# Performance work log

Measured on AMD Instinct MI355X. Metric: run time of the kernel, lower is better.

## Reference

```python
import jax, jax.numpy as jnp
import numpy as np

F_IN = 512
N_STAGES = 6
BATCH = 16384


def entmax15_1d(v):
    # Exact entmax with alpha=1.5 on a 1D vector (Peters et al. 2019).
    x = (v - jnp.max(v)) * 0.5
    xs = jnp.sort(x)[::-1]                      # descending
    rho = jnp.arange(1, xs.shape[0] + 1, dtype=xs.dtype)
    mean = jnp.cumsum(xs) / rho
    mean_sq = jnp.cumsum(xs * xs) / rho
    ss = rho * (mean_sq - mean * mean)
    delta = jnp.clip((1.0 - ss) / rho, 0.0, None)
    tau = mean - jnp.sqrt(delta)
    support_size = jnp.sum(tau <= xs)
    tau_star = tau[support_size - 1]
    return jnp.square(jnp.clip(x - tau_star, 0.0, None))


def setup_inputs() -> dict:
    key = jax.random.key(0)
    ks = jax.random.split(key, 7)
    F2 = 2 * F_IN
    lim_in = 1.0 / np.sqrt(F2)   # torch Linear default init bound (fan_in = 2F)
    x = jax.random.normal(ks[0], (BATCH, F_IN), dtype=jnp.float32)
    masks = jax.random.uniform(ks[1], (N_STAGES, F_IN), dtype=jnp.float32)  # Beta-sampled in torch; uniform(0,1) is in-range
    Win_w = jax.random.uniform(ks[2], (N_STAGES, F2, F2), minval=-lim_in, maxval=lim_in, dtype=jnp.float32)
    Win_b = jax.random.uniform(ks[3], (N_STAGES, F2), minval=-lim_in, maxval=lim_in, dtype=jnp.float32)
    Wout_w = jax.random.uniform(ks[4], (N_STAGES, F_IN, F2), minval=-lim_in, maxval=lim_in, dtype=jnp.float32)
    Wout_b = jax.random.uniform(ks[5], (N_STAGES, F_IN), minval=-lim_in, maxval=lim_in, dtype=jnp.float32)
    return {"x": x, "masks": masks, "Win_w": Win_w, "Win_b": Win_b,
            "Wout_w": Wout_w, "Wout_b": Wout_b}


def reference(x, masks, Win_w, Win_b, Wout_w, Wout_b):
    F = x.shape[-1]
    h = x
    for d in range(N_STAGES):
        feature = entmax15_1d(masks[d]) * x                      # [B, F]
        h_in = jnp.concatenate([feature, h], axis=-1) @ Win_w[d].T + Win_b[d]  # [B, 2F]
        z = jax.nn.sigmoid(h_in[:, :F])
        r = jax.nn.sigmoid(h_in[:, F:])
        h_out = jnp.tanh(jnp.concatenate([r * h, x], axis=-1) @ Wout_w[d].T + Wout_b[d])
        h = (1.0 - z) * h + z * h_out                            # dropout p=0 -> identity
    return h
```

## Files before the change

### kernel.cpp

```cpp
#include <hip/hip_runtime.h>
#include <stdint.h>
#include <math.h>

typedef unsigned short u16;
typedef short s16x8 __attribute__((ext_vector_type(8)));
typedef float f32x4 __attribute__((ext_vector_type(4)));
typedef u16 u16x4 __attribute__((ext_vector_type(4)));

#define FDIM 512
#define F2 1024
#define BATCH 16384
#define NST 6
#define KDIM 1024
#define NT 32

__device__ __forceinline__ u16 f2bf(float f) {
  uint32_t u = __float_as_uint(f);
  u += 0x7FFFu + ((u >> 16) & 1u);
  return (u16)(u >> 16);
}
__device__ __forceinline__ float bf2f(u16 b) {
  return __uint_as_float((uint32_t)b << 16);
}

#define LOG2E 1.44269504f
__device__ __forceinline__ float fast_sigmoid(float v) {
  float e = __builtin_amdgcn_exp2f(-v * LOG2E);
  return __builtin_amdgcn_rcpf(1.0f + e);
}
__device__ __forceinline__ float fast_tanh(float v) {
  float e = __builtin_amdgcn_exp2f(v * (2.0f * LOG2E));
  return 1.0f - 2.0f * __builtin_amdgcn_rcpf(1.0f + e);
}

__device__ __forceinline__ void ld_lds16(u16* lds, const u16* g) {
  __builtin_amdgcn_global_load_lds(
      (const __attribute__((address_space(1))) uint32_t*)g,
      (__attribute__((address_space(3))) uint32_t*)lds, 16, 0, 0);
}

__global__ __launch_bounds__(512) void entmax_kernel(const float* __restrict__ masks,
                                                     float* __restrict__ fm) {
  __shared__ float sx[FDIM];
  __shared__ float ssort[FDIM];
  __shared__ float stau[FDIM];
  __shared__ float2 sc[2][FDIM];
  const int d = blockIdx.x;
  const int j = threadIdx.x;
  float v = masks[d * FDIM + j];

  stau[j] = v;
  __syncthreads();
  for (int s = 256; s > 0; s >>= 1) {
    if (j < s) stau[j] = fmaxf(stau[j], stau[j + s]);
    __syncthreads();
  }
  float mx = stau[0];
  __syncthreads();

  float xx = (v - mx) * 0.5f;
  sx[j] = xx;
  __syncthreads();

  int r = 0;
  const float4* sx4 = (const float4*)sx;
#pragma unroll 4
  for (int i4 = 0; i4 < FDIM / 4; i4++) {
    float4 q = sx4[i4];
    int i = i4 << 2;
    r += (q.x > xx) || (q.x == xx && (i + 0) < j);
    r += (q.y > xx) || (q.y == xx && (i + 1) < j);
    r += (q.z > xx) || (q.z == xx && (i + 2) < j);
    r += (q.w > xx) || (q.w == xx && (i + 3) < j);
  }
  ssort[r] = xx;
  __syncthreads();
  float xs = ssort[j];

  sc[0][j] = make_float2(xs, xs * xs);
  __syncthreads();
  int pp = 0;
  for (int off = 1; off < FDIM; off <<= 1) {
    float2 t = sc[pp][j];
    if (j >= off) {
      float2 u = sc[pp][j - off];
      t.x += u.x;
      t.y += u.y;
    }
    sc[pp ^ 1][j] = t;
    __syncthreads();
    pp ^= 1;
  }
  float2 cs = sc[pp][j];

  float rho = (float)(j + 1);
  float mean = cs.x / rho;
  float msq = cs.y / rho;
  float ss = rho * (msq - mean * mean);
  float delta = (1.f - ss) / rho;
  if (delta < 0.f) delta = 0.f;
  float tau = mean - sqrtf(delta);
  stau[j] = tau;
  int cnt = __syncthreads_count(tau <= xs);
  float tstar = stau[cnt - 1];
  float c = fmaxf(xx - tstar, 0.f);
  fm[d * FDIM + j] = c * c;
}

__global__ __launch_bounds__(256) void cvt_w1_kernel(const float* __restrict__ src,
                                                     const float* __restrict__ fm,
                                                     u16* __restrict__ dst) {
  int t = blockIdx.x * 256 + threadIdx.x;
  int k = (t & 255) << 2;
  int dn = t >> 8;
  int d = dn >> 10;
  float4 v = *(const float4*)(src + (size_t)t * 4);
  if (k < FDIM) {
    float4 s = *(const float4*)(fm + (size_t)d * FDIM + k);
    v.x *= s.x; v.y *= s.y; v.z *= s.z; v.w *= s.w;
  }
  u16x4 o = {f2bf(v.x), f2bf(v.y), f2bf(v.z), f2bf(v.w)};
  *(u16x4*)(dst + (size_t)t * 4) = o;
}

__global__ __launch_bounds__(256) void cvt_kernel(const float* __restrict__ src,
                                                  u16* __restrict__ dst, int n4) {
  int t = blockIdx.x * blockDim.x + threadIdx.x;
  if (t >= n4) return;
  float4 v = *(const float4*)(src + (size_t)t * 4);
  u16x4 o = {f2bf(v.x), f2bf(v.y), f2bf(v.z), f2bf(v.w)};
  *(u16x4*)(dst + (size_t)t * 4) = o;
}

__global__ __launch_bounds__(256) void fill_xbf_kernel(const float* __restrict__ x,
                                                       u16* __restrict__ A1,
                                                       u16* __restrict__ A2) {
  int t = blockIdx.x * blockDim.x + threadIdx.x;
  int m = t >> 7;
  int c = (t & 127) << 2;
  float4 xv = *(const float4*)(x + (size_t)m * FDIM + c);
  u16x4 o = {f2bf(xv.x), f2bf(xv.y), f2bf(xv.z), f2bf(xv.w)};
  *(u16x4*)(A1 + (size_t)m * F2 + c) = o;
  *(u16x4*)(A1 + (size_t)m * F2 + FDIM + c) = o;
  *(u16x4*)(A2 + (size_t)m * F2 + FDIM + c) = o;
}

__device__ __forceinline__ void gemm_core128(const u16* __restrict__ Ag,
                                             const u16* __restrict__ Bg,
                                             int m0, int n0, u16* smem,
                                             f32x4 acc[4][4]) {
  const int tid = threadIdx.x;
  const int lane = tid & 63;
  const int wid = tid >> 6;
  const int wm = wid >> 1;
  const int wn = wid & 1;

  const int rs = tid >> 2;
  const int colsw = ((tid & 3) ^ ((rs >> 1) & 3)) << 3;
  const u16* gA0 = Ag + (size_t)(m0 + rs) * KDIM + colsw;
  const u16* gA1 = gA0 + (size_t)64 * KDIM;
  const u16* gB0 = Bg + (size_t)(n0 + rs) * KDIM + colsw;
  const u16* gB1 = gB0 + (size_t)64 * KDIM;
  const int lds_u = tid * 8;

  const int fcs = ((lane >> 4) ^ ((lane >> 1) & 3)) << 3;
  const int aoff = (wm * 64 + (lane & 15)) * 32 + fcs;
  const int boff = 4096 + (wn * 64 + (lane & 15)) * 32 + fcs;

#pragma unroll
  for (int i = 0; i < 4; i++)
#pragma unroll
    for (int j = 0; j < 4; j++) acc[i][j] = (f32x4){0.f, 0.f, 0.f, 0.f};

#pragma unroll
  for (int kt = 0; kt < 3; kt++) {
    u16* rb = smem + kt * 8192;
    ld_lds16(rb + lds_u, gA0 + kt * 32);
    ld_lds16(rb + 2048 + lds_u, gA1 + kt * 32);
    ld_lds16(rb + 4096 + lds_u, gB0 + kt * 32);
    ld_lds16(rb + 6144 + lds_u, gB1 + kt * 32);
  }
  asm volatile("s_waitcnt vmcnt(8)" ::: "memory");
  __builtin_amdgcn_s_barrier();
  __builtin_amdgcn_sched_barrier(0);

  for (int t = 0; t < NT; t++) {
    const u16* rb = smem + (t & 3) * 8192;
    u16* sb = smem + ((t + 3) & 3) * 8192;
    if (t + 3 < NT) {
      const int k0 = (t + 3) * 32;
      ld_lds16(sb + lds_u, gA0 + k0);
      ld_lds16(sb + 2048 + lds_u, gA1 + k0);
      ld_lds16(sb + 4096 + lds_u, gB0 + k0);
      ld_lds16(sb + 6144 + lds_u, gB1 + k0);
    }
    s16x8 af[4], bfr[4];
#pragma unroll
    for (int f = 0; f < 4; f++)
      af[f] = *(const s16x8*)(rb + aoff + f * 512);
#pragma unroll
    for (int g = 0; g < 4; g++)
      bfr[g] = *(const s16x8*)(rb + boff + g * 512);
    if (t < NT - 3) {
      asm volatile("s_waitcnt vmcnt(8)" ::: "memory");
    } else if (t == NT - 3) {
      asm volatile("s_waitcnt vmcnt(4)" ::: "memory");
    } else if (t == NT - 2) {
      asm volatile("s_waitcnt vmcnt(0)" ::: "memory");
    }
    __builtin_amdgcn_s_setprio(1);
#pragma unroll
    for (int f = 0; f < 4; f++)
#pragma unroll
      for (int g = 0; g < 4; g++)
        acc[f][g] = __builtin_amdgcn_mfma_f32_16x16x32_bf16(af[f], bfr[g], acc[f][g], 0, 0, 0);
    __builtin_amdgcn_s_setprio(0);
    __builtin_amdgcn_sched_barrier(0);
    __builtin_amdgcn_s_barrier();
    __builtin_amdgcn_sched_barrier(0);
  }
}

__global__ __launch_bounds__(256, 2) void gemm1_kernel(const u16* __restrict__ A1,
                                                       const u16* __restrict__ W1,
                                                       const float* __restrict__ b1,
                                                       _Float16* __restrict__ zbuf,
                                                       u16* __restrict__ A2) {
  __shared__ u16 smem[32768];
  const int bx = blockIdx.x;
  const int wg = (bx & 7) * 128 + (bx >> 3);
  const int m0 = (wg >> 3) << 7;
  const int n0 = (wg & 7) << 7;
  f32x4 acc[4][4];
  gemm_core128(A1, W1, m0, n0, smem, acc);

  const int lane = threadIdx.x & 63;
  const int wid = threadIdx.x >> 6;
  const int wm = wid >> 1;
  const int wn = wid & 1;
  const int fcol = lane & 15;
  const int frow = (lane >> 4) << 2;

  if (n0 < FDIM) {
#pragma unroll
    for (int f = 0; f < 4; f++)
#pragma unroll
      for (int g = 0; g < 4; g++)
#pragma unroll
        for (int r = 0; r < 4; r++) {
          int gm = m0 + wm * 64 + f * 16 + frow + r;
          int gn = n0 + wn * 64 + g * 16 + fcol;
          float v = acc[f][g][r] + b1[gn];
          zbuf[(size_t)gm * FDIM + gn] = (_Float16)fast_sigmoid(v);
        }
  } else {
#pragma unroll
    for (int f = 0; f < 4; f++)
#pragma unroll
      for (int g = 0; g < 4; g++)
#pragma unroll
        for (int r = 0; r < 4; r++) {
          int gm = m0 + wm * 64 + f * 16 + frow + r;
          int gn = n0 + wn * 64 + g * 16 + fcol;
          float v = acc[f][g][r] + b1[gn];
          float s = fast_sigmoid(v);
          int c = gn - FDIM;
          float h = bf2f(A1[(size_t)gm * F2 + FDIM + c]);
          A2[(size_t)gm * F2 + c] = f2bf(s * h);
        }
  }
}

__global__ __launch_bounds__(256, 2) void gemm2_kernel(const u16* __restrict__ A2,
                                                       const u16* __restrict__ W2,
                                                       const float* __restrict__ b2,
                                                       const _Float16* __restrict__ zbuf,
                                                       u16* __restrict__ A1,
                                                       float* __restrict__ out,
                                                       int last) {
  __shared__ u16 smem[32768];
  const int bx = blockIdx.x;
  const int wg = (bx & 7) * 64 + (bx >> 3);
  const int m0 = (wg >> 2) << 7;
  const int n0 = (wg & 3) << 7;
  f32x4 acc[4][4];
  gemm_core128(A2, W2, m0, n0, smem, acc);

  const int lane = threadIdx.x & 63;
  const int wid = threadIdx.x >> 6;
  const int wm = wid >> 1;
  const int wn = wid & 1;
  const int fcol = lane & 15;
  const int frow = (lane >> 4) << 2;

#pragma unroll
  for (int f = 0; f < 4; f++)
#pragma unroll
    for (int g = 0; g < 4; g++)
#pragma unroll
      for (int r = 0; r < 4; r++) {
        int gm = m0 + wm * 64 + f * 16 + frow + r;
        int gn = n0 + wn * 64 + g * 16 + fcol;
        float v = acc[f][g][r] + b2[gn];
        float ho = fast_tanh(v);
        size_t idx = (size_t)gm * FDIM + gn;
        float z = (float)zbuf[idx];
        float hv = bf2f(A1[(size_t)gm * F2 + FDIM + gn]);
        float hn = (1.0f - z) * hv + z * ho;
        if (last)
          out[idx] = hn;
        else
          A1[(size_t)gm * F2 + FDIM + gn] = f2bf(hn);
      }
}

extern "C" void kernel_launch(void* const* d_in, const int* in_sizes, int n_in,
                              void* d_out, int out_size, void* d_ws, size_t ws_size,
                              hipStream_t stream) {
  (void)in_sizes; (void)n_in; (void)out_size; (void)ws_size;
  const float* x = (const float*)d_in[0];
  const float* masks = (const float*)d_in[1];
  const float* W1f = (const float*)d_in[2];
  const float* b1 = (const float*)d_in[3];
  const float* W2f = (const float*)d_in[4];
  const float* b2 = (const float*)d_in[5];

  char* ws = (char*)d_ws;
  float* fm = (float*)ws;       ws += (size_t)NST * FDIM * 4;
  u16* W1b = (u16*)ws;          ws += (size_t)NST * F2 * F2 * 2;
  u16* W2b = (u16*)ws;          ws += (size_t)NST * FDIM * F2 * 2;
  u16* A1 = (u16*)ws;           ws += (size_t)BATCH * F2 * 2;
  u16* A2 = (u16*)ws;           ws += (size_t)BATCH * F2 * 2;
  _Float16* zbuf = (_Float16*)ws; ws += (size_t)BATCH * FDIM * 2;
  float* out = (float*)d_out;

  entmax_kernel<<<NST, 512, 0, stream>>>(masks, fm);
  cvt_w1_kernel<<<NST * F2 * F2 / 4 / 256, 256, 0, stream>>>(W1f, fm, W1b);
  {
    int n4 = NST * FDIM * F2 / 4;
    cvt_kernel<<<(n4 + 255) / 256, 256, 0, stream>>>(W2f, W2b, n4);
  }
  fill_xbf_kernel<<<BATCH * 128 / 256, 256, 0, stream>>>(x, A1, A2);

  for (int d = 0; d < NST; d++) {
    gemm1_kernel<<<(BATCH / 128) * (F2 / 128), 256, 0, stream>>>(
        A1, W1b + (size_t)d * F2 * F2, b1 + d * F2, zbuf, A2);
    gemm2_kernel<<<(BATCH / 128) * (FDIM / 128), 256, 0, stream>>>(
        A2, W2b + (size_t)d * FDIM * F2, b2 + d * FDIM, zbuf,
        A1, out, d == NST - 1);
  }
}
```

Baseline: 542.1 us.

## Load A operand directly into registers, halve LDS, raise occupancy

The shared GEMM core stops staging the A tile through LDS. Each wave now loads its A fragments straight from global memory into a 4-deep register ring, two k-steps ahead, while only the B tile keeps the LDS pipeline. This halves shared memory per block and raises the launch bound to three blocks per CU, aiming to cut LDS traffic and hide latency with more waves. The cost is more register pressure, which may cause spilling at the higher occupancy. The A global loads are also less coalesced and no longer shared between the two waves that use the same rows, and the vmcnt accounting gets more complex.

```diff
diff --git a/kernel.cpp b/kernel.cpp
--- a/kernel.cpp
+++ b/kernel.cpp
@@ -157,15 +157,16 @@
 
   const int rs = tid >> 2;
   const int colsw = ((tid & 3) ^ ((rs >> 1) & 3)) << 3;
-  const u16* gA0 = Ag + (size_t)(m0 + rs) * KDIM + colsw;
-  const u16* gA1 = gA0 + (size_t)64 * KDIM;
   const u16* gB0 = Bg + (size_t)(n0 + rs) * KDIM + colsw;
   const u16* gB1 = gB0 + (size_t)64 * KDIM;
   const int lds_u = tid * 8;
 
   const int fcs = ((lane >> 4) ^ ((lane >> 1) & 3)) << 3;
-  const int aoff = (wm * 64 + (lane & 15)) * 32 + fcs;
-  const int boff = 4096 + (wn * 64 + (lane & 15)) * 32 + fcs;
+  const int boff = (wn * 64 + (lane & 15)) * 32 + fcs;
+
+  const u16* gA = Ag + (size_t)(m0 + wm * 64 + (lane & 15)) * KDIM + ((lane >> 4) << 3);
+
+  s16x8 ar[4][4];
 
 #pragma unroll
   for (int i = 0; i < 4; i++)
@@ -174,38 +175,46 @@
 
 #pragma unroll
   for (int kt = 0; kt < 3; kt++) {
-    u16* rb = smem + kt * 8192;
-    ld_lds16(rb + lds_u, gA0 + kt * 32);
-    ld_lds16(rb + 2048 + lds_u, gA1 + kt * 32);
-    ld_lds16(rb + 4096 + lds_u, gB0 + kt * 32);
-    ld_lds16(rb + 6144 + lds_u, gB1 + kt * 32);
-  }
-  asm volatile("s_waitcnt vmcnt(8)" ::: "memory");
+    u16* rb = smem + kt * 4096;
+    ld_lds16(rb + lds_u, gB0 + kt * 32);
+    ld_lds16(rb + 2048 + lds_u, gB1 + kt * 32);
+  }
+  __builtin_amdgcn_sched_barrier(0);
+#pragma unroll
+  for (int kt = 0; kt < 2; kt++)
+#pragma unroll
+    for (int f = 0; f < 4; f++)
+      ar[kt][f] = *(const s16x8*)(gA + (size_t)f * 16 * KDIM + kt * 32);
+  asm volatile("s_waitcnt vmcnt(4)" ::: "memory");
   __builtin_amdgcn_s_barrier();
   __builtin_amdgcn_sched_barrier(0);
 
+#pragma unroll
   for (int t = 0; t < NT; t++) {
-    const u16* rb = smem + (t & 3) * 8192;
-    u16* sb = smem + ((t + 3) & 3) * 8192;
     if (t + 3 < NT) {
-      const int k0 = (t + 3) * 32;
-      ld_lds16(sb + lds_u, gA0 + k0);
-      ld_lds16(sb + 2048 + lds_u, gA1 + k0);
-      ld_lds16(sb + 4096 + lds_u, gB0 + k0);
-      ld_lds16(sb + 6144 + lds_u, gB1 + k0);
+      u16* sb = smem + ((t + 3) & 3) * 4096;
+      ld_lds16(sb + lds_u, gB0 + (t + 3) * 32);
+      ld_lds16(sb + 2048 + lds_u, gB1 + (t + 3) * 32);
     }
-    s16x8 af[4], bfr[4];
-#pragma unroll
-    for (int f = 0; f < 4; f++)
-      af[f] = *(const s16x8*)(rb + aoff + f * 512);
+    __builtin_amdgcn_sched_barrier(0);
+    if (t + 2 < NT) {
+#pragma unroll
+      for (int f = 0; f < 4; f++)
+        ar[(t + 2) & 3][f] =
+            *(const s16x8*)(gA + (size_t)f * 16 * KDIM + (t + 2) * 32);
+    }
+    const u16* rb = smem + (t & 3) * 4096;
+    s16x8 bfr[4];
 #pragma unroll
     for (int g = 0; g < 4; g++)
       bfr[g] = *(const s16x8*)(rb + boff + g * 512);
     if (t < NT - 3) {
-      asm volatile("s_waitcnt vmcnt(8)" ::: "memory");
+      asm volatile("s_waitcnt vmcnt(12)" ::: "memory");
     } else if (t == NT - 3) {
+      asm volatile("s_waitcnt vmcnt(10)" ::: "memory");
+    } else if (t == NT - 2) {
       asm volatile("s_waitcnt vmcnt(4)" ::: "memory");
-    } else if (t == NT - 2) {
+    } else {
       asm volatile("s_waitcnt vmcnt(0)" ::: "memory");
     }
     __builtin_amdgcn_s_setprio(1);
@@ -213,7 +222,8 @@
     for (int f = 0; f < 4; f++)
 #pragma unroll
       for (int g = 0; g < 4; g++)
-        acc[f][g] = __builtin_amdgcn_mfma_f32_16x16x32_bf16(af[f], bfr[g], acc[f][g], 0, 0, 0);
+        acc[f][g] = __builtin_amdgcn_mfma_f32_16x16x32_bf16(ar[t & 3][f], bfr[g],
+                                                            acc[f][g], 0, 0, 0);
     __builtin_amdgcn_s_setprio(0);
     __builtin_amdgcn_sched_barrier(0);
     __builtin_amdgcn_s_barrier();
@@ -221,12 +231,12 @@
   }
 }
 
-__global__ __launch_bounds__(256, 2) void gemm1_kernel(const u16* __restrict__ A1,
+__global__ __launch_bounds__(256, 3) void gemm1_kernel(const u16* __restrict__ A1,
                                                        const u16* __restrict__ W1,
                                                        const float* __restrict__ b1,
                                                        _Float16* __restrict__ zbuf,
                                                        u16* __restrict__ A2) {
-  __shared__ u16 smem[32768];
+  __shared__ u16 smem[16384];
   const int bx = blockIdx.x;
   const int wg = (bx & 7) * 128 + (bx >> 3);
   const int m0 = (wg >> 3) << 7;
@@ -271,14 +281,14 @@
   }
 }
 
-__global__ __launch_bounds__(256, 2) void gemm2_kernel(const u16* __restrict__ A2,
+__global__ __launch_bounds__(256, 3) void gemm2_kernel(const u16* __restrict__ A2,
                                                        const u16* __restrict__ W2,
                                                        const float* __restrict__ b2,
                                                        const _Float16* __restrict__ zbuf,
                                                        u16* __restrict__ A1,
                                                        float* __restrict__ out,
                                                        int last) {
-  __shared__ u16 smem[32768];
+  __shared__ u16 smem[16384];
   const int bx = blockIdx.x;
   const int wg = (bx & 7) * 64 + (bx >> 3);
   const int m0 = (wg >> 2) << 7;
```

Result: slower. 822.2 us (+51.7%).
